# Performance work log

Measured on AMD Instinct MI355X. Metric: run time of the kernel, lower is better.

The kernel has to match this reference:

```python
import jax, jax.numpy as jnp
import numpy as np

MARGIN = 0.5  # init kwarg 'margin'
TWO_N, D = 8192, 256


def setup_inputs() -> dict:
    key = jax.random.key(0)
    k1, k2 = jax.random.split(key)
    embeddings = jax.random.normal(k1, (TWO_N, D), dtype=jnp.float32)
    neg_mask = jax.random.bernoulli(k2, 0.5, (TWO_N, TWO_N))  # bool [2N, 2N]
    return {"embeddings": embeddings, "neg_mask": neg_mask}


def _cdist(x, y):
    # Euclidean pairwise distances via the Gram trick (matches torch.cdist p=2)
    x2 = jnp.sum(x * x, axis=-1)[:, None]
    y2 = jnp.sum(y * y, axis=-1)[None, :]
    sq = jnp.maximum(x2 + y2 - 2.0 * (x @ y.T), 0.0)
    return jnp.sqrt(sq + 1e-12)


def reference(embeddings, neg_mask):
    two_n = embeddings.shape[0]
    n = two_n // 2
    d = _cdist(embeddings, embeddings)  # [2N, 2N]
    # masked sum of exp(margin - d) per anchor row (vectorizes the python loop)
    exp_neg = jnp.where(neg_mask, jnp.exp(MARGIN - d), 0.0)
    row_sums = exp_neg.sum(axis=1)  # [2N]
    idx = jnp.arange(n)
    ap = d[idx, idx + n]  # anchor-positive distances [N]
    j = jnp.log(row_sums[:n] + row_sums[n:]) + ap  # [N]
    # original skips NaN entries before the mean
    valid = ~jnp.isnan(j)
    r2 = jnp.where(valid, jnp.square(jnp.maximum(j, 0.0)), 0.0)
    cnt = jnp.maximum(valid.sum(), 1).astype(r2.dtype)
    loss = r2.sum() / cnt / 2.0
    return loss
```

## Files before the change

### kernel.cpp

```cpp
#include <hip/hip_runtime.h>
#include <hip/hip_bf16.h>
#include <stdint.h>

#define TWO_N  8192
#define NHALF  4096
#define DDIM   256
#define MARGIN 0.5f

static const size_t OFF_EMB  = 0;
static const size_t OFF_X2   = 4u * 1024 * 1024;
static const size_t OFF_AP   = OFF_X2 + (size_t)TWO_N * 4;
static const size_t OFF_FLAG = OFF_AP + (size_t)NHALF * 4;
static const size_t OFF_PART = OFF_FLAG + 256;
static const size_t OFF_RS   = OFF_PART + 64ull * TWO_N * 4;

typedef __attribute__((ext_vector_type(8))) short bf16x8;
typedef __attribute__((ext_vector_type(4))) float f32x4;

__device__ inline ushort f2bf(float f) {
  uint32_t u = __float_as_uint(f);
  uint32_t r = (u + 0x7FFFu + ((u >> 16) & 1u)) >> 16;
  return (ushort)r;
}
__device__ inline float bf2f(ushort h) { return __uint_as_float((uint32_t)h << 16); }

__device__ inline void gload_lds16(const void* g, void* l) {
  __builtin_amdgcn_global_load_lds(
      (const __attribute__((address_space(1))) uint32_t*)(uintptr_t)g,
      (__attribute__((address_space(3))) uint32_t*)(uint32_t)(uintptr_t)l,
      16, 0, 0);
}

__global__ __launch_bounds__(256) void smv2_prep(
    const float* __restrict__ emb,
    const uint32_t* __restrict__ maskw,
    ushort* __restrict__ emb_bf,
    float* __restrict__ x2,
    int* __restrict__ flag)
{
  const int t = threadIdx.x;
  if (blockIdx.x == 0) {
    __shared__ int sflag;
    if (t == 0) sflag = 0;
    __syncthreads();
    int found = 0;
    #pragma unroll
    for (int k = 0; k < 8; ++k) {
      uint32_t w = maskw[t * 8 + k];
      if (w > 1u && (w & 0xFEFEFEFEu) == 0u) found = 1;
    }
    if (found) atomicOr(&sflag, 1);
    __syncthreads();
    if (t == 0) *flag = sflag;
  }
  const int row  = blockIdx.x * 8 + (t >> 5);
  const int lane = t & 31;
  const float* rp = emb + (size_t)row * DDIM + lane * 8;
  float4 v0 = *(const float4*)(rp);
  float4 v1 = *(const float4*)(rp + 4);
  float vals[8] = {v0.x, v0.y, v0.z, v0.w, v1.x, v1.y, v1.z, v1.w};
  uint32_t packed[4];
  float ss = 0.f;
  #pragma unroll
  for (int k = 0; k < 4; ++k) {
    ushort h0 = f2bf(vals[2 * k]);
    ushort h1 = f2bf(vals[2 * k + 1]);
    packed[k] = (uint32_t)h0 | ((uint32_t)h1 << 16);
    float f0 = bf2f(h0), f1 = bf2f(h1);
    ss += f0 * f0 + f1 * f1;
  }
  *(uint4*)(emb_bf + (size_t)row * DDIM + lane * 8) =
      make_uint4(packed[0], packed[1], packed[2], packed[3]);
  #pragma unroll
  for (int m = 1; m < 32; m <<= 1) ss += __shfl_xor(ss, m);
  if (lane == 0) x2[row] = ss;
}

__global__ __launch_bounds__(512, 4) void smv2_main(
    const ushort* __restrict__ emb_bf,
    const float* __restrict__ x2,
    const uint8_t* __restrict__ mask8,
    const int* __restrict__ flagp,
    float* __restrict__ ap,
    float* __restrict__ partial)
{
  __shared__ char ldsAB[2][32768];
  __shared__ uint8_t ldsM[128 * 128];

  const int t = threadIdx.x;

  const int bid = blockIdx.x;
  const int xcd = bid & 7;
  const int idx = bid >> 3;
  const int bx  = xcd * 8 + (idx & 7);
  const int by  = idx >> 3;
  const int brow = by * 128;
  const int bcol = bx * 128;

  const char* gA = (const char*)(emb_bf + (size_t)brow * DDIM);
  const char* gB = (const char*)(emb_bf + (size_t)bcol * DDIM);

  #pragma unroll
  for (int it = 0; it < 2; ++it) {
    const int dl   = it * 8192 + t * 16;
    const int mrow = dl >> 7;
    const int mc   = dl & 127;
    const int msw  = ((mrow >> 2) & 3) << 5;
    gload_lds16(mask8 + (size_t)(brow + mrow) * TWO_N + bcol + (mc ^ msw), ldsM + dl);
  }

  #pragma unroll
  for (int it = 0; it < 2; ++it) {
    const int dl  = it * 8192 + t * 16;
    const int row = dl >> 7;
    const int c   = dl & 127;
    const int cb  = c ^ ((row & 7) << 4);
    gload_lds16(gA + (size_t)row * 512 + 0 * 128 + cb, ldsAB[0] + dl);
    gload_lds16(gB + (size_t)row * 512 + 0 * 128 + cb, ldsAB[0] + 16384 + dl);
  }
  __syncthreads();

  const int w  = t >> 6;
  const int l  = t & 63;
  const int wr = w >> 2;
  const int wc = w & 3;
  const int cl = l & 15;
  const int kh = l >> 4;
  const int swz = (cl & 7) << 4;

  f32x4 acc[4][2];
  #pragma unroll
  for (int m = 0; m < 4; ++m)
    #pragma unroll
    for (int n = 0; n < 2; ++n) {
      f32x4 z = {0.f, 0.f, 0.f, 0.f};
      acc[m][n] = z;
    }

  #pragma unroll
  for (int p = 0; p < 4; ++p) {
    if (p < 3) {
      char* dst = ldsAB[(p + 1) & 1];
      #pragma unroll
      for (int it = 0; it < 2; ++it) {
        const int dl  = it * 8192 + t * 16;
        const int row = dl >> 7;
        const int c   = dl & 127;
        const int cb  = c ^ ((row & 7) << 4);
        gload_lds16(gA + (size_t)row * 512 + (p + 1) * 128 + cb, dst + dl);
        gload_lds16(gB + (size_t)row * 512 + (p + 1) * 128 + cb, dst + 16384 + dl);
      }
    }
    __builtin_amdgcn_sched_barrier(0);

    const char* buf = ldsAB[p & 1];
    #pragma unroll
    for (int ks = 0; ks < 2; ++ks) {
      const int kb = ks * 64 + kh * 16;
      bf16x8 a[4], b[2];
      #pragma unroll
      for (int m = 0; m < 4; ++m)
        a[m] = *(const bf16x8*)(buf + (wr * 64 + m * 16 + cl) * 128 + (kb ^ swz));
      #pragma unroll
      for (int n = 0; n < 2; ++n)
        b[n] = *(const bf16x8*)(buf + 16384 + (wc * 32 + n * 16 + cl) * 128 + (kb ^ swz));
      #pragma unroll
      for (int m = 0; m < 4; ++m)
        #pragma unroll
        for (int n = 0; n < 2; ++n)
          acc[m][n] = __builtin_amdgcn_mfma_f32_16x16x32_bf16(a[m], b[n], acc[m][n], 0, 0, 0);
    }
    __syncthreads();
  }

  float* part = (float*)ldsAB[0];
  const int isByte = *flagp;
  const uint32_t* maskww = (const uint32_t*)mask8;

  float x2j[2];
  #pragma unroll
  for (int n = 0; n < 2; ++n) x2j[n] = x2[bcol + wc * 32 + n * 16 + cl];

  #pragma unroll
  for (int m = 0; m < 4; ++m) {
    #pragma unroll
    for (int q = 0; q < 4; ++q) {
      const int lrow = wr * 64 + m * 16 + kh * 4 + q;
      const int gi = brow + lrow;
      const float xi = x2[gi];
      const int msw = ((lrow >> 2) & 3) << 5;
      float rp = 0.f;
      #pragma unroll
      for (int n = 0; n < 2; ++n) {
        const int jc = wc * 32 + n * 16 + cl;
        const int gj = bcol + jc;
        const float g = acc[m][n][q];
        float sq = (gi == gj) ? 0.f : (xi + x2j[n] - 2.f * g);
        sq = fmaxf(sq, 0.f) + 1e-12f;
        const float dd = sqrtf(sq);
        if (gj == gi + NHALF && gi < NHALF) ap[gi] = dd;
        bool mk;
        if (isByte) mk = ldsM[lrow * 128 + (jc ^ msw)] != 0;
        else        mk = maskww[(size_t)gi * TWO_N + gj] != 0u;
        rp += mk ? __expf(MARGIN - dd) : 0.f;
      }
      #pragma unroll
      for (int s = 1; s < 16; s <<= 1) rp += __shfl_xor(rp, s);
      if (cl == 0) part[wc * 128 + lrow] = rp;
    }
  }
  __syncthreads();
  if (t < 128) {
    partial[(size_t)bx * TWO_N + brow + t] =
        (part[t] + part[128 + t]) + (part[256 + t] + part[384 + t]);
  }
}

__global__ __launch_bounds__(256) void smv2_rowsum(
    const float* __restrict__ partial, float* __restrict__ rs)
{
  const int row = blockIdx.x * 256 + threadIdx.x;
  float s = 0.f;
  #pragma unroll 8
  for (int b = 0; b < 64; ++b) s += partial[(size_t)b * TWO_N + row];
  rs[row] = s;
}

__global__ __launch_bounds__(1024) void smv2_finalize(
    const float* __restrict__ rs, const float* __restrict__ ap,
    float* __restrict__ out)
{
  const int t = threadIdx.x;
  float sum = 0.f, cnt = 0.f;
  for (int i = t; i < NHALF; i += 1024) {
    float rsum = rs[i] + rs[i + NHALF];
    float jv = logf(rsum) + ap[i];
    if (!isnan(jv)) {
      cnt += 1.f;
      float mj = fmaxf(jv, 0.f);
      sum += mj * mj;
    }
  }
  __shared__ float ssum[16], scnt[16];
  #pragma unroll
  for (int s = 32; s >= 1; s >>= 1) {
    sum += __shfl_down(sum, s);
    cnt += __shfl_down(cnt, s);
  }
  const int wid = t >> 6, lid = t & 63;
  if (lid == 0) { ssum[wid] = sum; scnt[wid] = cnt; }
  __syncthreads();
  if (t == 0) {
    float S = 0.f, C = 0.f;
    #pragma unroll
    for (int i = 0; i < 16; ++i) { S += ssum[i]; C += scnt[i]; }
    if (C < 1.f) C = 1.f;
    out[0] = S / C * 0.5f;
  }
}

extern "C" void kernel_launch(void* const* d_in, const int* in_sizes, int n_in,
                              void* d_out, int out_size, void* d_ws, size_t ws_size,
                              hipStream_t stream) {
  const float* emb = (const float*)d_in[0];
  const void* mask = d_in[1];
  char* ws = (char*)d_ws;

  ushort* emb_bf = (ushort*)(ws + OFF_EMB);
  float*  x2     = (float*)(ws + OFF_X2);
  float*  ap     = (float*)(ws + OFF_AP);
  int*    flag   = (int*)(ws + OFF_FLAG);
  float*  part   = (float*)(ws + OFF_PART);
  float*  rs     = (float*)(ws + OFF_RS);

  smv2_prep<<<1024, 256, 0, stream>>>(emb, (const uint32_t*)mask, emb_bf, x2, flag);
  smv2_main<<<4096, 512, 0, stream>>>(emb_bf, x2, (const uint8_t*)mask, flag, ap, part);
  smv2_rowsum<<<32, 256, 0, stream>>>(part, rs);
  smv2_finalize<<<1, 1024, 0, stream>>>(rs, ap, (float*)d_out);
}
```

Before: 513.6 us.

## Exploit distance-matrix symmetry: compute only upper-triangle tiles, accumulate column sums

The main kernel now launches only the 2080 upper-triangular 128x128 tiles instead of all 4096. Each off-diagonal tile reuses its exp(margin - d) values for the transposed block, reading the transposed mask directly from global memory and writing column partial sums into the mirror block's partial row. The double-buffered LDS pipeline becomes a single buffer to reduce LDS use and raise occupancy, and x2 is staged in LDS. This roughly halves the GEMM and exp work, at the cost of strided transposed-mask global reads and lost load/compute overlap.

```diff
diff --git a/kernel.cpp b/kernel.cpp
--- a/kernel.cpp
+++ b/kernel.cpp
@@ -6,6 +6,7 @@
 #define NHALF  4096
 #define DDIM   256
 #define MARGIN 0.5f
+#define NTRI   2080
 
 static const size_t OFF_EMB  = 0;
 static const size_t OFF_X2   = 4u * 1024 * 1024;
@@ -76,7 +77,7 @@
   if (lane == 0) x2[row] = ss;
 }
 
-__global__ __launch_bounds__(512, 4) void smv2_main(
+__global__ __launch_bounds__(512, 6) void smv2_main(
     const ushort* __restrict__ emb_bf,
     const float* __restrict__ x2,
     const uint8_t* __restrict__ mask8,
@@ -84,18 +85,23 @@
     float* __restrict__ ap,
     float* __restrict__ partial)
 {
-  __shared__ char ldsAB[2][32768];
+  __shared__ char ldsA[128 * 128];
+  __shared__ char ldsB[128 * 128];
   __shared__ uint8_t ldsM[128 * 128];
+  __shared__ float ldsX[256];
 
   const int t = threadIdx.x;
 
   const int bid = blockIdx.x;
-  const int xcd = bid & 7;
-  const int idx = bid >> 3;
-  const int bx  = xcd * 8 + (idx & 7);
-  const int by  = idx >> 3;
+  const int idx = (bid & 7) * (NTRI / 8) + (bid >> 3);
+  float rf = sqrtf(8.f * (float)idx + 1.f);
+  int bx = (int)((rf - 1.f) * 0.5f);
+  while ((bx + 1) * (bx + 2) / 2 <= idx) ++bx;
+  while (bx * (bx + 1) / 2 > idx) --bx;
+  const int by = idx - bx * (bx + 1) / 2;
   const int brow = by * 128;
   const int bcol = bx * 128;
+  const bool diag = (bx == by);
 
   const char* gA = (const char*)(emb_bf + (size_t)brow * DDIM);
   const char* gB = (const char*)(emb_bf + (size_t)bcol * DDIM);
@@ -108,15 +114,18 @@
     const int msw  = ((mrow >> 2) & 3) << 5;
     gload_lds16(mask8 + (size_t)(brow + mrow) * TWO_N + bcol + (mc ^ msw), ldsM + dl);
   }
-
+  if (t < 64) {
+    const float* src = (t < 32) ? (x2 + brow + t * 4) : (x2 + bcol + (t - 32) * 4);
+    gload_lds16(src, (char*)ldsX + t * 16);
+  }
   #pragma unroll
   for (int it = 0; it < 2; ++it) {
     const int dl  = it * 8192 + t * 16;
     const int row = dl >> 7;
     const int c   = dl & 127;
     const int cb  = c ^ ((row & 7) << 4);
-    gload_lds16(gA + (size_t)row * 512 + 0 * 128 + cb, ldsAB[0] + dl);
-    gload_lds16(gB + (size_t)row * 512 + 0 * 128 + cb, ldsAB[0] + 16384 + dl);
+    gload_lds16(gA + (size_t)row * 512 + cb, ldsA + dl);
+    gload_lds16(gB + (size_t)row * 512 + cb, ldsB + dl);
   }
   __syncthreads();
 
@@ -139,47 +148,54 @@
 
   #pragma unroll
   for (int p = 0; p < 4; ++p) {
+    #pragma unroll
+    for (int ks = 0; ks < 2; ++ks) {
+      const int kb = ks * 64 + kh * 16;
+      bf16x8 a[4], b[2];
+      #pragma unroll
+      for (int m = 0; m < 4; ++m)
+        a[m] = *(const bf16x8*)(ldsA + (wr * 64 + m * 16 + cl) * 128 + (kb ^ swz));
+      #pragma unroll
+      for (int n = 0; n < 2; ++n)
+        b[n] = *(const bf16x8*)(ldsB + (wc * 32 + n * 16 + cl) * 128 + (kb ^ swz));
+      #pragma unroll
+      for (int m = 0; m < 4; ++m)
+        #pragma unroll
+        for (int n = 0; n < 2; ++n)
+          acc[m][n] = __builtin_amdgcn_mfma_f32_16x16x32_bf16(a[m], b[n], acc[m][n], 0, 0, 0);
+    }
+    __syncthreads();
     if (p < 3) {
-      char* dst = ldsAB[(p + 1) & 1];
       #pragma unroll
       for (int it = 0; it < 2; ++it) {
         const int dl  = it * 8192 + t * 16;
         const int row = dl >> 7;
         const int c   = dl & 127;
         const int cb  = c ^ ((row & 7) << 4);
-        gload_lds16(gA + (size_t)row * 512 + (p + 1) * 128 + cb, dst + dl);
-        gload_lds16(gB + (size_t)row * 512 + (p + 1) * 128 + cb, dst + 16384 + dl);
+        gload_lds16(gA + (size_t)row * 512 + (p + 1) * 128 + cb, ldsA + dl);
+        gload_lds16(gB + (size_t)row * 512 + (p + 1) * 128 + cb, ldsB + dl);
       }
-    }
-    __builtin_amdgcn_sched_barrier(0);
-
-    const char* buf = ldsAB[p & 1];
-    #pragma unroll
-    for (int ks = 0; ks < 2; ++ks) {
-      const int kb = ks * 64 + kh * 16;
-      bf16x8 a[4], b[2];
-      #pragma unroll
-      for (int m = 0; m < 4; ++m)
-        a[m] = *(const bf16x8*)(buf + (wr * 64 + m * 16 + cl) * 128 + (kb ^ swz));
-      #pragma unroll
-      for (int n = 0; n < 2; ++n)
-        b[n] = *(const bf16x8*)(buf + 16384 + (wc * 32 + n * 16 + cl) * 128 + (kb ^ swz));
-      #pragma unroll
-      for (int m = 0; m < 4; ++m)
-        #pragma unroll
-        for (int n = 0; n < 2; ++n)
-          acc[m][n] = __builtin_amdgcn_mfma_f32_16x16x32_bf16(a[m], b[n], acc[m][n], 0, 0, 0);
-    }
-    __syncthreads();
-  }
-
-  float* part = (float*)ldsAB[0];
+      __syncthreads();
+    }
+  }
+
   const int isByte = *flagp;
   const uint32_t* maskww = (const uint32_t*)mask8;
 
-  float x2j[2];
-  #pragma unroll
-  for (int n = 0; n < 2; ++n) x2j[n] = x2[bcol + wc * 32 + n * 16 + cl];
+  uint32_t m2r[2][4];
+  if (!diag && isByte) {
+    #pragma unroll
+    for (int n = 0; n < 2; ++n) {
+      const int gj = bcol + wc * 32 + n * 16 + cl;
+      #pragma unroll
+      for (int m = 0; m < 4; ++m)
+        m2r[n][m] = *(const uint32_t*)(mask8 + (size_t)gj * TWO_N + brow + wr * 64 + m * 16 + kh * 4);
+    }
+  }
+
+  float* part  = (float*)ldsA;
+  float* part2 = (float*)ldsB;
+  float cs[2] = {0.f, 0.f};
 
   #pragma unroll
   for (int m = 0; m < 4; ++m) {
@@ -187,32 +203,51 @@
     for (int q = 0; q < 4; ++q) {
       const int lrow = wr * 64 + m * 16 + kh * 4 + q;
       const int gi = brow + lrow;
-      const float xi = x2[gi];
-      const int msw = ((lrow >> 2) & 3) << 5;
+      const float xi = ldsX[lrow];
+      const int msw = kh << 5;
       float rp = 0.f;
       #pragma unroll
       for (int n = 0; n < 2; ++n) {
         const int jc = wc * 32 + n * 16 + cl;
         const int gj = bcol + jc;
         const float g = acc[m][n][q];
-        float sq = (gi == gj) ? 0.f : (xi + x2j[n] - 2.f * g);
+        float sq = (gi == gj) ? 0.f : (xi + ldsX[128 + jc] - 2.f * g);
         sq = fmaxf(sq, 0.f) + 1e-12f;
         const float dd = sqrtf(sq);
         if (gj == gi + NHALF && gi < NHALF) ap[gi] = dd;
-        bool mk;
-        if (isByte) mk = ldsM[lrow * 128 + (jc ^ msw)] != 0;
-        else        mk = maskww[(size_t)gi * TWO_N + gj] != 0u;
-        rp += mk ? __expf(MARGIN - dd) : 0.f;
+        const float e = __expf(MARGIN - dd);
+        bool mk1;
+        if (isByte) mk1 = ldsM[lrow * 128 + (jc ^ msw)] != 0;
+        else        mk1 = maskww[(size_t)gi * TWO_N + gj] != 0u;
+        rp += mk1 ? e : 0.f;
+        if (!diag) {
+          bool mk2;
+          if (isByte) mk2 = ((m2r[n][m] >> (8 * q)) & 255u) != 0u;
+          else        mk2 = maskww[(size_t)gj * TWO_N + gi] != 0u;
+          cs[n] += mk2 ? e : 0.f;
+        }
       }
       #pragma unroll
       for (int s = 1; s < 16; s <<= 1) rp += __shfl_xor(rp, s);
       if (cl == 0) part[wc * 128 + lrow] = rp;
     }
   }
+
+  if (!diag) {
+    #pragma unroll
+    for (int n = 0; n < 2; ++n) {
+      cs[n] += __shfl_xor(cs[n], 16);
+      cs[n] += __shfl_xor(cs[n], 32);
+      if (l < 16) part2[wr * 128 + wc * 32 + n * 16 + l] = cs[n];
+    }
+  }
   __syncthreads();
+
   if (t < 128) {
     partial[(size_t)bx * TWO_N + brow + t] =
         (part[t] + part[128 + t]) + (part[256 + t] + part[384 + t]);
+    if (!diag)
+      partial[(size_t)by * TWO_N + bcol + t] = part2[t] + part2[128 + t];
   }
 }
 
@@ -274,7 +309,7 @@
   float*  rs     = (float*)(ws + OFF_RS);
 
   smv2_prep<<<1024, 256, 0, stream>>>(emb, (const uint32_t*)mask, emb_bf, x2, flag);
-  smv2_main<<<4096, 512, 0, stream>>>(emb_bf, x2, (const uint8_t*)mask, flag, ap, part);
+  smv2_main<<<NTRI, 512, 0, stream>>>(emb_bf, x2, (const uint8_t*)mask, flag, ap, part);
   smv2_rowsum<<<32, 256, 0, stream>>>(part, rs);
   smv2_finalize<<<1, 1024, 0, stream>>>(rs, ap, (float*)d_out);
 }
```

Result: faster. 455.6 us (-11.3%).
